# Kernel tuning notes

Measured on AMD Instinct MI355X. Metric: run time of the kernel, lower is better.

The kernel has to match this reference:

```python
import jax, jax.numpy as jnp
import numpy as np

N, S, E = 8, 1024, 768
H = 12
D = E // H  # head_dim = 64
FF = 4 * E
EPS = 1e-5


def setup_inputs() -> dict:
    key = jax.random.key(0)
    ks = jax.random.split(key, 12)
    s = lambda fan_in: 1.0 / np.sqrt(fan_in)
    return {
        "x": jax.random.normal(ks[0], (N, S, E), dtype=jnp.float32),
        "ln1_g": jnp.ones((E,), jnp.float32),
        "ln1_b": jnp.zeros((E,), jnp.float32),
        "ln2_g": jnp.ones((E,), jnp.float32),
        "ln2_b": jnp.zeros((E,), jnp.float32),
        "w_attn": jax.random.normal(ks[1], (E, 3 * E), jnp.float32) * s(E),
        "b_attn": jax.random.normal(ks[2], (3 * E,), jnp.float32) * 0.02,
        "w_proj": jax.random.normal(ks[3], (E, E), jnp.float32) * s(E),
        "b_proj": jax.random.normal(ks[4], (E,), jnp.float32) * 0.02,
        "w_fc": jax.random.normal(ks[5], (E, FF), jnp.float32) * s(E),
        "b_fc": jax.random.normal(ks[6], (FF,), jnp.float32) * 0.02,
        "w_fc2": jax.random.normal(ks[7], (FF, E), jnp.float32) * s(FF),
        "b_fc2": jax.random.normal(ks[8], (E,), jnp.float32) * 0.02,
    }


def _layernorm(x, g, b):
    mu = jnp.mean(x, axis=-1, keepdims=True)
    var = jnp.var(x, axis=-1, keepdims=True)
    return (x - mu) * jax.lax.rsqrt(var + EPS) * g + b


def reference(x, ln1_g, ln1_b, ln2_g, ln2_b, w_attn, b_attn, w_proj, b_proj,
              w_fc, b_fc, w_fc2, b_fc2):
    # --- attention branch (pre-LN) ---
    h = _layernorm(x, ln1_g, ln1_b)
    qkv = h @ w_attn + b_attn                       # [N,S,3E]
    q, k, v = jnp.split(qkv, 3, axis=-1)
    q = q.reshape(N, S, H, D).transpose(0, 2, 1, 3)  # [N,H,S,D]
    k = k.reshape(N, S, H, D).transpose(0, 2, 1, 3)
    v = v.reshape(N, S, H, D).transpose(0, 2, 1, 3)
    attn = jnp.einsum('nhsd,nhtd->nhst', q, k) * (1.0 / np.sqrt(D))
    causal = jnp.tril(jnp.ones((S, S), bool))
    attn = jnp.where(causal, attn, -jnp.inf)
    p = jax.nn.softmax(attn, axis=-1)
    out = jnp.einsum('nhst,nhtd->nhsd', p, v)        # [N,H,S,D]
    out = out.transpose(0, 2, 1, 3).reshape(N, S, E)
    x = x + (out @ w_proj + b_proj)
    # --- MLP branch ---
    h2 = _layernorm(x, ln2_g, ln2_b)
    ff = jax.nn.gelu(h2 @ w_fc + b_fc, approximate=False)  # exact GELU (torch nn.GELU default)
    x = x + (ff @ w_fc2 + b_fc2)
    return x
```

## Files before the change

kernel.cpp:

```cpp
#include <hip/hip_runtime.h>
#include <hip/hip_bf16.h>
#include <stdint.h>

#define S_LEN 1024
#define E_DIM 768
#define H_N   12
#define FF_DIM 3072

typedef __hip_bfloat16 bf16;
using short8  = __attribute__((ext_vector_type(8))) short;
using short4v = __attribute__((ext_vector_type(4))) short;
using f32x4   = __attribute__((ext_vector_type(4))) float;

__device__ __forceinline__ void async_cp16(const void* g, void* l) {
  __builtin_amdgcn_global_load_lds(
      (__attribute__((address_space(1))) void*)(g),
      (__attribute__((address_space(3))) void*)(l), 16, 0, 0);
}

__global__ __launch_bounds__(256) void wcastT_all(
    const float* __restrict__ wa, const float* __restrict__ wp,
    const float* __restrict__ wf, const float* __restrict__ wf2,
    bf16* __restrict__ oa, bf16* __restrict__ op,
    bf16* __restrict__ of, bf16* __restrict__ of2) {
  __shared__ float t[32][33];
  int bid = blockIdx.x;
  const float* w; bf16* wt; int K, N, bx, by;
  if (bid < 1728)      { w = wa;  wt = oa;  K = 768;  N = 2304; int r = bid;        bx = r % 72; by = r / 72; }
  else if (bid < 2304) { w = wp;  wt = op;  K = 768;  N = 768;  int r = bid - 1728; bx = r % 24; by = r / 24; }
  else if (bid < 4608) { w = wf;  wt = of;  K = 768;  N = 3072; int r = bid - 2304; bx = r % 96; by = r / 96; }
  else                 { w = wf2; wt = of2; K = 3072; N = 768;  int r = bid - 4608; bx = r % 24; by = r / 24; }
  int x = threadIdx.x & 31;
  int y = threadIdx.x >> 5;
  for (int i = y; i < 32; i += 8)
    t[i][x] = w[(size_t)(by * 32 + i) * N + bx * 32 + x];
  __syncthreads();
  for (int i = y; i < 32; i += 8)
    wt[(size_t)(bx * 32 + i) * K + by * 32 + x] = __float2bfloat16(t[x][i]);
}

__global__ __launch_bounds__(256) void ln_rows(const float* __restrict__ x,
                                               const float* __restrict__ g,
                                               const float* __restrict__ b,
                                               bf16* __restrict__ out) {
  int row = blockIdx.x;
  int tid = threadIdx.x;
  const float* xr = x + (size_t)row * E_DIM;
  float v0 = xr[tid], v1 = xr[tid + 256], v2 = xr[tid + 512];
  float s = v0 + v1 + v2;
  float ss = v0 * v0 + v1 * v1 + v2 * v2;
  for (int o = 32; o > 0; o >>= 1) {
    s  += __shfl_down(s, o);
    ss += __shfl_down(ss, o);
  }
  __shared__ float ps[4], pq[4];
  int wv = tid >> 6;
  if ((tid & 63) == 0) { ps[wv] = s; pq[wv] = ss; }
  __syncthreads();
  s  = ps[0] + ps[1] + ps[2] + ps[3];
  ss = pq[0] + pq[1] + pq[2] + pq[3];
  float mu  = s * (1.0f / E_DIM);
  float var = ss * (1.0f / E_DIM) - mu * mu;
  float rs  = rsqrtf(var + 1e-5f);
  bf16* orow = out + (size_t)row * E_DIM;
  orow[tid]       = __float2bfloat16((v0 - mu) * rs * g[tid]       + b[tid]);
  orow[tid + 256] = __float2bfloat16((v1 - mu) * rs * g[tid + 256] + b[tid + 256]);
  orow[tid + 512] = __float2bfloat16((v2 - mu) * rs * g[tid + 512] + b[tid + 512]);
}

template <int MODE>
__global__ __launch_bounds__(256) void gemm_bt(
    const bf16* __restrict__ A, const bf16* __restrict__ Bt,
    const float* __restrict__ bias, const float* __restrict__ resid,
    float* __restrict__ outf, bf16* __restrict__ ob0, bf16* __restrict__ ob1,
    bf16* __restrict__ ob2, int M, int N, int K) {
  __shared__ bf16 As[2][128 * 64];
  __shared__ bf16 Bs[2][128 * 64];
  int tid = threadIdx.x;
  int wave = tid >> 6, lane = tid & 63;
  int quad = lane >> 4, l16 = lane & 15;
  int gx = N >> 7;
  int flat = blockIdx.x;
  int y8 = flat & 7;
  int q2 = flat >> 3;
  int bx = q2 % gx;
  int by = (q2 / gx) * 8 + y8;
  int m0 = by * 128, n0 = bx * 128;
  int wm = (wave & 1) * 64, wn = (wave >> 1) * 64;
  f32x4 acc[4][4];
  for (int i = 0; i < 4; i++)
    for (int j = 0; j < 4; j++)
      for (int r = 0; r < 4; r++) acc[i][j][r] = 0.f;

  int xs = l16 & 7;
  int srow = tid >> 3;
  int scg = (((tid & 7) ^ (srow & 7)) << 3);
  const bf16* aptr = A  + (size_t)(m0 + srow) * K + scg;
  const bf16* bptr = Bt + (size_t)(n0 + srow) * K + scg;
  int ldst = tid * 8;

#pragma unroll
  for (int t = 0; t < 4; t++) {
    async_cp16(aptr + (size_t)t * 32 * K, &As[0][ldst + t * 2048]);
    async_cp16(bptr + (size_t)t * 32 * K, &Bs[0][ldst + t * 2048]);
  }
  int nkb = K >> 6;
  for (int ik = 0; ik < nkb; ++ik) {
    int cur = ik & 1;
    if (ik + 1 < nkb) {
      size_t ko = (size_t)(ik + 1) * 64;
#pragma unroll
      for (int t = 0; t < 4; t++) {
        async_cp16(aptr + ko + (size_t)t * 32 * K, &As[cur ^ 1][ldst + t * 2048]);
        async_cp16(bptr + ko + (size_t)t * 32 * K, &Bs[cur ^ 1][ldst + t * 2048]);
      }
      asm volatile("s_waitcnt vmcnt(8)" ::: "memory");
    } else {
      asm volatile("s_waitcnt vmcnt(0)" ::: "memory");
    }
    __builtin_amdgcn_s_barrier();
    asm volatile("" ::: "memory");
#pragma unroll
    for (int ks = 0; ks < 2; ks++) {
      int ko2 = (((ks * 4 + quad) ^ xs) << 3);
      short8 af[4], bfr[4];
      for (int i = 0; i < 4; i++)
        af[i] = *(const short8*)&As[cur][(wm + i * 16 + l16) * 64 + ko2];
      for (int j = 0; j < 4; j++)
        bfr[j] = *(const short8*)&Bs[cur][(wn + j * 16 + l16) * 64 + ko2];
      for (int i = 0; i < 4; i++)
        for (int j = 0; j < 4; j++)
          acc[i][j] = __builtin_amdgcn_mfma_f32_16x16x32_bf16(
              bfr[j], af[i], acc[i][j], 0, 0, 0);
    }
    asm volatile("" ::: "memory");
    __builtin_amdgcn_s_barrier();
  }

  for (int j = 0; j < 4; j++) {
    int colb = n0 + wn + j * 16 + quad * 4;
    f32x4 b4 = *(const f32x4*)&bias[colb];
    for (int i = 0; i < 4; i++) {
      int row = m0 + wm + i * 16 + l16;
      f32x4 v = acc[i][j] + b4;
      if (MODE == 0) {
        int nn = row >> 10, s = row & 1023;
        if (colb < 768) {
          int h = colb >> 6, db = colb & 63;
          short4v pk;
          for (int r = 0; r < 4; r++)
            pk[r] = __builtin_bit_cast(short, __float2bfloat16(v[r] * 0.125f));
          *(short4v*)&ob0[(((size_t)nn * H_N + h) * S_LEN + s) * 64 + db] = pk;
        } else if (colb < 1536) {
          int c = colb - 768;
          size_t nh2 = (size_t)nn * H_N + (c >> 6);
          int d = c & 63;
          short4v pk;
          for (int r = 0; r < 4; r++)
            pk[r] = __builtin_bit_cast(short, __float2bfloat16(v[r]));
          *(short4v*)&ob1[((nh2 * 8 + (d >> 3)) * S_LEN + s) * 8 + (d & 7)] = pk;
        } else {
          int c = colb - 1536;
          size_t nh2 = (size_t)nn * H_N + (c >> 6);
          int d0 = c & 63;
          for (int r = 0; r < 4; r++)
            ob2[((nh2 * 128 + (s >> 3)) * 64 + d0 + r) * 8 + (s & 7)] =
                __float2bfloat16(v[r]);
        }
      } else if (MODE == 2) {
        short4v pk;
        for (int r = 0; r < 4; r++) {
          float x = v[r];
          float t = x * (1.59576912161f + 0.0713548162726f * x * x);
          float g = x * __builtin_amdgcn_rcpf(1.0f + __expf(-t));
          pk[r] = __builtin_bit_cast(short, __float2bfloat16(g));
        }
        *(short4v*)&ob0[(size_t)row * N + colb] = pk;
      }
    }
  }
}

__global__ __launch_bounds__(256) void gemm_bt64(
    const bf16* __restrict__ A, const bf16* __restrict__ Bt,
    const float* __restrict__ bias, const float* __restrict__ resid,
    float* __restrict__ outf, int M, int N, int K) {
  __shared__ bf16 As[2][128 * 64];
  __shared__ bf16 Bs[2][64 * 64];
  int tid = threadIdx.x;
  int wave = tid >> 6, lane = tid & 63;
  int quad = lane >> 4, l16 = lane & 15;
  int gx = N >> 6;
  int flat = blockIdx.x;
  int y8 = flat & 7;
  int q2 = flat >> 3;
  int bx = q2 % gx;
  int by = (q2 / gx) * 8 + y8;
  int m0 = by * 128, n0 = bx * 64;
  int wm = wave * 32;
  f32x4 acc[2][4];
  for (int i = 0; i < 2; i++)
    for (int j = 0; j < 4; j++)
      for (int r = 0; r < 4; r++) acc[i][j][r] = 0.f;

  int xs = l16 & 7;
  int srow = tid >> 3;
  int scg = (((tid & 7) ^ (srow & 7)) << 3);
  const bf16* aptr = A  + (size_t)(m0 + srow) * K + scg;
  const bf16* bptr = Bt + (size_t)(n0 + srow) * K + scg;
  int ldst = tid * 8;

#pragma unroll
  for (int t = 0; t < 4; t++)
    async_cp16(aptr + (size_t)t * 32 * K, &As[0][ldst + t * 2048]);
#pragma unroll
  for (int t = 0; t < 2; t++)
    async_cp16(bptr + (size_t)t * 32 * K, &Bs[0][ldst + t * 2048]);

  int nkb = K >> 6;
  for (int ik = 0; ik < nkb; ++ik) {
    int cur = ik & 1;
    if (ik + 1 < nkb) {
      size_t ko = (size_t)(ik + 1) * 64;
#pragma unroll
      for (int t = 0; t < 4; t++)
        async_cp16(aptr + ko + (size_t)t * 32 * K, &As[cur ^ 1][ldst + t * 2048]);
#pragma unroll
      for (int t = 0; t < 2; t++)
        async_cp16(bptr + ko + (size_t)t * 32 * K, &Bs[cur ^ 1][ldst + t * 2048]);
      asm volatile("s_waitcnt vmcnt(6)" ::: "memory");
    } else {
      asm volatile("s_waitcnt vmcnt(0)" ::: "memory");
    }
    __builtin_amdgcn_s_barrier();
    asm volatile("" ::: "memory");
#pragma unroll
    for (int ks = 0; ks < 2; ks++) {
      int ko2 = (((ks * 4 + quad) ^ xs) << 3);
      short8 af[2], bfr[4];
      for (int i = 0; i < 2; i++)
        af[i] = *(const short8*)&As[cur][(wm + i * 16 + l16) * 64 + ko2];
      for (int j = 0; j < 4; j++)
        bfr[j] = *(const short8*)&Bs[cur][(j * 16 + l16) * 64 + ko2];
      for (int i = 0; i < 2; i++)
        for (int j = 0; j < 4; j++)
          acc[i][j] = __builtin_amdgcn_mfma_f32_16x16x32_bf16(
              bfr[j], af[i], acc[i][j], 0, 0, 0);
    }
    asm volatile("" ::: "memory");
    __builtin_amdgcn_s_barrier();
  }

  for (int j = 0; j < 4; j++) {
    int colb = n0 + j * 16 + quad * 4;
    f32x4 b4 = *(const f32x4*)&bias[colb];
    for (int i = 0; i < 2; i++) {
      int row = m0 + wm + i * 16 + l16;
      size_t idx = (size_t)row * N + colb;
      f32x4 rv = *(const f32x4*)&resid[idx];
      *(f32x4*)&outf[idx] = acc[i][j] + b4 + rv;
    }
  }
}

__global__ __launch_bounds__(256) void attn_fwd(
    const bf16* __restrict__ q, const bf16* __restrict__ kg,
    const bf16* __restrict__ vg, bf16* __restrict__ out) {
  __shared__ bf16 kt2[2][8 * 64 * 8];
  __shared__ bf16 vt2[2][8 * 64 * 8];
  __shared__ bf16 pba[4][16 * 68];
  __shared__ bf16 pbb[4][16 * 68];
  int flat = blockIdx.x;
  int xcd = flat & 7;
  int j = flat >> 3;
  int a = j & 7;
  int g = j >> 3;
  int nh = xcd * 12 + g;
  int b = 15 - a;
  int n = nh / H_N, h = nh % H_N;
  int tid = threadIdx.x, wave = tid >> 6, lane = tid & 63;
  int quad = lane >> 4, l16 = lane & 15;
  const bf16* qp = q  + (size_t)nh * S_LEN * 64;
  const bf16* kp = kg + (size_t)nh * 8 * S_LEN * 8;
  const bf16* vp = vg + (size_t)nh * 128 * 64 * 8;
  int qra = a * 64 + wave * 16;
  int qrb = b * 64 + wave * 16;

  short8 qfa[2], qfb[2];
  qfa[0] = *(const short8*)&qp[(size_t)(qra + l16) * 64 + quad * 8];
  qfa[1] = *(const short8*)&qp[(size_t)(qra + l16) * 64 + 32 + quad * 8];
  qfb[0] = *(const short8*)&qp[(size_t)(qrb + l16) * 64 + quad * 8];
  qfb[1] = *(const short8*)&qp[(size_t)(qrb + l16) * 64 + 32 + quad * 8];

  const bf16* kbase = kp + (((size_t)(tid >> 6) * S_LEN) + (tid & 63)) * 8;
  const bf16* vbase = vp + (((size_t)(tid >> 6) * 64) + (tid & 63)) * 8;

  f32x4 oaa[4], oab[4];
  for (int dt = 0; dt < 4; dt++)
    for (int r = 0; r < 4; r++) { oaa[dt][r] = 0.f; oab[dt][r] = 0.f; }
  float lia = 0.f, lib = 0.f;

  {
    bf16* lk = &kt2[0][0] + tid * 8;
    bf16* lv = &vt2[0][0] + tid * 8;
#pragma unroll
    for (int t = 0; t < 2; ++t) {
      async_cp16(kbase + (size_t)t * 4 * S_LEN * 8, lk + t * 2048);
      async_cp16(vbase + (size_t)t * 2048, lv + t * 2048);
    }
  }

  for (int kb = 0; kb <= b; ++kb) {
    bool act_a = (kb <= a);
    int cur = kb & 1;
    __syncthreads();

    short8 kf[2][4], vf[2][4];
#pragma unroll
    for (int ks = 0; ks < 2; ks++)
      for (int nt = 0; nt < 4; nt++) {
        kf[ks][nt] = *(const short8*)
            &kt2[cur][(size_t)((ks * 4 + quad) * 64 + nt * 16 + l16) * 8];
        vf[ks][nt] = *(const short8*)
            &vt2[cur][(size_t)((ks * 4 + quad) * 64 + nt * 16 + l16) * 8];
      }
    if (kb < b) {
      bf16* lk = &kt2[cur ^ 1][0] + tid * 8;
      bf16* lv = &vt2[cur ^ 1][0] + tid * 8;
      size_t kko = (size_t)(kb + 1) * 512;
      size_t vko = (size_t)(kb + 1) * 4096;
#pragma unroll
      for (int t = 0; t < 2; ++t) {
        async_cp16(kbase + kko + (size_t)t * 4 * S_LEN * 8, lk + t * 2048);
        async_cp16(vbase + vko + (size_t)t * 2048, lv + t * 2048);
      }
    }

    f32x4 sb4[4], sa4[4];
    for (int nt = 0; nt < 4; nt++) {
      for (int r = 0; r < 4; r++) { sb4[nt][r] = -10.f; sa4[nt][r] = -10.f; }
      for (int ks = 0; ks < 2; ks++) {
        sb4[nt] = __builtin_amdgcn_mfma_f32_16x16x32_bf16(kf[ks][nt], qfb[ks],
                                                          sb4[nt], 0, 0, 0);
        if (act_a)
          sa4[nt] = __builtin_amdgcn_mfma_f32_16x16x32_bf16(kf[ks][nt], qfa[ks],
                                                            sa4[nt], 0, 0, 0);
      }
    }
    if (kb == b) {
      int ql = wave * 16 + l16;
      for (int nt = 0; nt < 4; nt++)
        for (int r = 0; r < 4; r++)
          if (nt * 16 + quad * 4 + r > ql) sb4[nt][r] = -INFINITY;
    }
    if (kb == a) {
      int ql = wave * 16 + l16;
      for (int nt = 0; nt < 4; nt++)
        for (int r = 0; r < 4; r++)
          if (nt * 16 + quad * 4 + r > ql) sa4[nt][r] = -INFINITY;
    }

    float rsb = 0.f;
    for (int nt = 0; nt < 4; nt++)
      for (int r = 0; r < 4; r++) {
        float p = __expf(sb4[nt][r]);
        sb4[nt][r] = p;
        rsb += p;
      }
    rsb += __shfl_xor(rsb, 16);
    rsb += __shfl_xor(rsb, 32);
    lib += rsb;
    bf16* pwb = pbb[wave];
    for (int nt = 0; nt < 4; nt++) {
      short4v pk;
      for (int r = 0; r < 4; r++)
        pk[r] = __builtin_bit_cast(short, __float2bfloat16(sb4[nt][r]));
      *(short4v*)&pwb[l16 * 68 + nt * 16 + quad * 4] = pk;
    }
    if (act_a) {
      float rsa = 0.f;
      for (int nt = 0; nt < 4; nt++)
        for (int r = 0; r < 4; r++) {
          float p = __expf(sa4[nt][r]);
          sa4[nt][r] = p;
          rsa += p;
        }
      rsa += __shfl_xor(rsa, 16);
      rsa += __shfl_xor(rsa, 32);
      lia += rsa;
      bf16* pwa = pba[wave];
      for (int nt = 0; nt < 4; nt++) {
        short4v pk;
        for (int r = 0; r < 4; r++)
          pk[r] = __builtin_bit_cast(short, __float2bfloat16(sa4[nt][r]));
        *(short4v*)&pwa[l16 * 68 + nt * 16 + quad * 4] = pk;
      }
    }
    asm volatile("s_waitcnt lgkmcnt(0)" ::: "memory");

    for (int ks = 0; ks < 2; ks++) {
      short8 pfb = *(const short8*)&pbb[wave][l16 * 68 + ks * 32 + quad * 8];
      short8 pfa;
      if (act_a) pfa = *(const short8*)&pba[wave][l16 * 68 + ks * 32 + quad * 8];
      for (int dt = 0; dt < 4; dt++) {
        oab[dt] = __builtin_amdgcn_mfma_f32_16x16x32_bf16(vf[ks][dt], pfb,
                                                          oab[dt], 0, 0, 0);
        if (act_a)
          oaa[dt] = __builtin_amdgcn_mfma_f32_16x16x32_bf16(vf[ks][dt], pfa,
                                                            oaa[dt], 0, 0, 0);
      }
    }
  }

  float inva = 1.0f / lia, invb = 1.0f / lib;
  int ta = n * S_LEN + qra + l16;
  int tb = n * S_LEN + qrb + l16;
  for (int dt = 0; dt < 4; dt++) {
    short4v ova, ovb;
    for (int r = 0; r < 4; r++) {
      ova[r] = __builtin_bit_cast(short, __float2bfloat16(oaa[dt][r] * inva));
      ovb[r] = __builtin_bit_cast(short, __float2bfloat16(oab[dt][r] * invb));
    }
    *(short4v*)&out[(size_t)ta * E_DIM + h * 64 + dt * 16 + quad * 4] = ova;
    *(short4v*)&out[(size_t)tb * E_DIM + h * 64 + dt * 16 + quad * 4] = ovb;
  }
}

extern "C" void kernel_launch(void* const* d_in, const int* in_sizes, int n_in,
                              void* d_out, int out_size, void* d_ws, size_t ws_size,
                              hipStream_t stream) {
  (void)in_sizes; (void)n_in; (void)out_size; (void)ws_size;
  const float* x      = (const float*)d_in[0];
  const float* ln1_g  = (const float*)d_in[1];
  const float* ln1_b  = (const float*)d_in[2];
  const float* ln2_g  = (const float*)d_in[3];
  const float* ln2_b  = (const float*)d_in[4];
  const float* w_attn = (const float*)d_in[5];
  const float* b_attn = (const float*)d_in[6];
  const float* w_proj = (const float*)d_in[7];
  const float* b_proj = (const float*)d_in[8];
  const float* w_fc   = (const float*)d_in[9];
  const float* b_fc   = (const float*)d_in[10];
  const float* w_fc2  = (const float*)d_in[11];
  const float* b_fc2  = (const float*)d_in[12];
  float* out = (float*)d_out;

  char* ws = (char*)d_ws;
  bf16* wt_attn = (bf16*)(ws);
  bf16* wt_proj = (bf16*)(ws + 3538944);
  bf16* wt_fc   = (bf16*)(ws + 4718592);
  bf16* wt_fc2  = (bf16*)(ws + 9437184);
  bf16* hbuf    = (bf16*)(ws + 14155776);
  float* x2     = (float*)(ws + 26738688);
  bf16* qb      = (bf16*)(ws + 51904512);
  bf16* kbuf    = (bf16*)(ws + 64487424);
  bf16* vtb     = (bf16*)(ws + 77070336);
  bf16* ao      = (bf16*)(ws + 89653248);
  bf16* ff      = qb;

  dim3 blk(256);
  wcastT_all<<<dim3(6912), blk, 0, stream>>>(w_attn, w_proj, w_fc, w_fc2,
                                             wt_attn, wt_proj, wt_fc, wt_fc2);

  ln_rows<<<8192, blk, 0, stream>>>(x, ln1_g, ln1_b, hbuf);

  gemm_bt<0><<<dim3(18 * 64), blk, 0, stream>>>(
      hbuf, wt_attn, b_attn, nullptr, nullptr, qb, kbuf, vtb, 8192, 2304, 768);

  attn_fwd<<<dim3(768), blk, 0, stream>>>(qb, kbuf, vtb, ao);

  gemm_bt64<<<dim3(12 * 64), blk, 0, stream>>>(
      ao, wt_proj, b_proj, x, x2, 8192, 768, 768);

  ln_rows<<<8192, blk, 0, stream>>>(x2, ln2_g, ln2_b, hbuf);

  gemm_bt<2><<<dim3(24 * 64), blk, 0, stream>>>(
      hbuf, wt_fc, b_fc, nullptr, nullptr, ff, nullptr, nullptr, 8192, 3072, 768);

  gemm_bt64<<<dim3(12 * 64), blk, 0, stream>>>(
      ff, wt_fc2, b_fc2, x2, out, 8192, 768, 3072);
}
```

Baseline: 349.3 us.

## Replace QKV and FC1 GEMMs with 256x256-tile 8-wave ping-pong pipelined kernel

The 128x128 4-wave GEMM used for the QKV and FC1 projections is replaced by a 256x256-tile kernel with 512 threads. Each wave computes a 128x64 sub-tile. The K loop is split into quarter-tile phases that interleave LDS fragment loads, async global-to-LDS prefetch of the next K slices, and MFMA bursts under raised priority. The larger tile increases data reuse per LDS byte and the schedule is meant to overlap memory with compute. The cost is more barriers, higher register pressure from 128 accumulators per lane, and fewer blocks, 288 and 384, across the CUs.

```diff
diff --git a/kernel.cpp b/kernel.cpp
--- a/kernel.cpp
+++ b/kernel.cpp
@@ -69,80 +69,132 @@
 }
 
 template <int MODE>
-__global__ __launch_bounds__(256) void gemm_bt(
+__global__ __launch_bounds__(512, 2) void gemm8(
     const bf16* __restrict__ A, const bf16* __restrict__ Bt,
-    const float* __restrict__ bias, const float* __restrict__ resid,
-    float* __restrict__ outf, bf16* __restrict__ ob0, bf16* __restrict__ ob1,
-    bf16* __restrict__ ob2, int M, int N, int K) {
-  __shared__ bf16 As[2][128 * 64];
-  __shared__ bf16 Bs[2][128 * 64];
+    const float* __restrict__ bias,
+    bf16* __restrict__ ob0, bf16* __restrict__ ob1, bf16* __restrict__ ob2,
+    int M, int N, int K) {
+  __shared__ bf16 lA[2][16384];
+  __shared__ bf16 lB[2][16384];
   int tid = threadIdx.x;
-  int wave = tid >> 6, lane = tid & 63;
+  int w = tid >> 6, lane = tid & 63;
   int quad = lane >> 4, l16 = lane & 15;
-  int gx = N >> 7;
+  int wr = w >> 2, wc = w & 3;
+  int gx = N >> 8;
   int flat = blockIdx.x;
   int y8 = flat & 7;
   int q2 = flat >> 3;
   int bx = q2 % gx;
   int by = (q2 / gx) * 8 + y8;
-  int m0 = by * 128, n0 = bx * 128;
-  int wm = (wave & 1) * 64, wn = (wave >> 1) * 64;
-  f32x4 acc[4][4];
-  for (int i = 0; i < 4; i++)
+  int m0 = by << 8, n0 = bx << 8;
+
+  f32x4 acc[8][4];
+#pragma unroll
+  for (int i = 0; i < 8; i++)
+#pragma unroll
     for (int j = 0; j < 4; j++)
+#pragma unroll
       for (int r = 0; r < 4; r++) acc[i][j][r] = 0.f;
 
   int xs = l16 & 7;
-  int srow = tid >> 3;
-  int scg = (((tid & 7) ^ (srow & 7)) << 3);
-  const bf16* aptr = A  + (size_t)(m0 + srow) * K + scg;
-  const bf16* bptr = Bt + (size_t)(n0 + srow) * K + scg;
-  int ldst = tid * 8;
-
-#pragma unroll
-  for (int t = 0; t < 4; t++) {
-    async_cp16(aptr + (size_t)t * 32 * K, &As[0][ldst + t * 2048]);
-    async_cp16(bptr + (size_t)t * 32 * K, &Bs[0][ldst + t * 2048]);
-  }
-  int nkb = K >> 6;
-  for (int ik = 0; ik < nkb; ++ik) {
-    int cur = ik & 1;
-    if (ik + 1 < nkb) {
-      size_t ko = (size_t)(ik + 1) * 64;
-#pragma unroll
-      for (int t = 0; t < 4; t++) {
-        async_cp16(aptr + ko + (size_t)t * 32 * K, &As[cur ^ 1][ldst + t * 2048]);
-        async_cp16(bptr + ko + (size_t)t * 32 * K, &Bs[cur ^ 1][ldst + t * 2048]);
-      }
-      asm volatile("s_waitcnt vmcnt(8)" ::: "memory");
-    } else {
-      asm volatile("s_waitcnt vmcnt(0)" ::: "memory");
-    }
-    __builtin_amdgcn_s_barrier();
-    asm volatile("" ::: "memory");
-#pragma unroll
-    for (int ks = 0; ks < 2; ks++) {
-      int ko2 = (((ks * 4 + quad) ^ xs) << 3);
-      short8 af[4], bfr[4];
-      for (int i = 0; i < 4; i++)
-        af[i] = *(const short8*)&As[cur][(wm + i * 16 + l16) * 64 + ko2];
-      for (int j = 0; j < 4; j++)
-        bfr[j] = *(const short8*)&Bs[cur][(wn + j * 16 + l16) * 64 + ko2];
-      for (int i = 0; i < 4; i++)
-        for (int j = 0; j < 4; j++)
-          acc[i][j] = __builtin_amdgcn_mfma_f32_16x16x32_bf16(
-              bfr[j], af[i], acc[i][j], 0, 0, 0);
-    }
-    asm volatile("" ::: "memory");
-    __builtin_amdgcn_s_barrier();
-  }
-
-  for (int j = 0; j < 4; j++) {
-    int colb = n0 + wn + j * 16 + quad * 4;
+  int ko0 = (quad ^ xs) << 3;
+  int ko1 = ((4 + quad) ^ xs) << 3;
+  int sgo = ((tid & 7) ^ ((tid >> 3) & 7)) << 3;
+  size_t aRB = (size_t)(m0 + (tid >> 3)) * K + sgo;
+  size_t bRB = (size_t)(n0 + ((tid >> 8) << 6) + ((tid >> 3) & 31)) * K + sgo;
+  int aD = tid * 8;
+  int bD = ((tid >> 8) << 12) + (tid & 255) * 8;
+
+  auto stA = [&](int buf, int mh, int kt) {
+#pragma unroll
+    for (int p = 0; p < 2; ++p)
+      async_cp16(A + aRB + (size_t)(mh * 64 + p * 128) * K + (size_t)kt * 64,
+                 &lA[buf][aD + mh * 4096 + p * 8192]);
+  };
+  auto stB = [&](int buf, int nh, int kt) {
+#pragma unroll
+    for (int p = 0; p < 2; ++p)
+      async_cp16(Bt + bRB + (size_t)(nh * 32 + p * 128) * K + (size_t)kt * 64,
+                 &lB[buf][bD + nh * 2048 + p * 8192]);
+  };
+
+  short8 af[4][2], b0f[2][2], b1f[2][2];
+
+#define LD_A(BUF, MH)                                                      \
+  {                                                                        \
+    _Pragma("unroll") for (int i = 0; i < 4; ++i) {                        \
+      const bf16* bp = &lA[BUF][(wr * 128 + (MH)*64 + i * 16 + l16) * 64]; \
+      af[i][0] = *(const short8*)&bp[ko0];                                 \
+      af[i][1] = *(const short8*)&bp[ko1];                                 \
+    }                                                                      \
+  }
+#define LD_B(BUF, NH, DST)                                                 \
+  {                                                                        \
+    _Pragma("unroll") for (int j = 0; j < 2; ++j) {                        \
+      const bf16* bp = &lB[BUF][(wc * 64 + (NH)*32 + j * 16 + l16) * 64];  \
+      DST[j][0] = *(const short8*)&bp[ko0];                                \
+      DST[j][1] = *(const short8*)&bp[ko1];                                \
+    }                                                                      \
+  }
+#define DO_MFMA(MH, NH, BSRC)                                              \
+  {                                                                        \
+    __builtin_amdgcn_s_setprio(1);                                         \
+    _Pragma("unroll") for (int ks = 0; ks < 2; ++ks)                       \
+        _Pragma("unroll") for (int i = 0; i < 4; ++i)                      \
+            _Pragma("unroll") for (int j = 0; j < 2; ++j)                  \
+                acc[(MH)*4 + i][(NH)*2 + j] =                              \
+        __builtin_amdgcn_mfma_f32_16x16x32_bf16(                           \
+            BSRC[j][ks], af[i][ks], acc[(MH)*4 + i][(NH)*2 + j], 0, 0, 0); \
+    __builtin_amdgcn_s_setprio(0);                                         \
+  }
+#define BAR() __builtin_amdgcn_s_barrier()
+#define LGKM0() asm volatile("s_waitcnt lgkmcnt(0)" ::: "memory")
+#define VM6() asm volatile("s_waitcnt vmcnt(6)" ::: "memory")
+#define VM0() asm volatile("s_waitcnt vmcnt(0)" ::: "memory")
+
+  stA(0, 0, 0); stA(0, 1, 0); stB(0, 0, 0); stB(0, 1, 0);
+  stA(1, 0, 1); stB(1, 1, 1); stA(1, 1, 1);
+  VM6();
+  BAR();
+
+  int nit = K >> 7;
+  for (int it = 0; it < nit; ++it) {
+    int kt1 = 2 * it + 1, ktA = 2 * it + 2, ktB = 2 * it + 3;
+    bool more = (it + 1 < nit);
+    LD_A(0, 0); LD_B(0, 0, b0f);
+    stB(1, 0, kt1);
+    BAR(); LGKM0(); DO_MFMA(0, 0, b0f); BAR();
+    LD_B(0, 1, b1f);
+    if (more) stA(0, 0, ktA);
+    BAR(); LGKM0(); DO_MFMA(0, 1, b1f); BAR();
+    LD_A(0, 1);
+    if (more) stB(0, 1, ktA);
+    BAR(); LGKM0(); DO_MFMA(1, 1, b1f); BAR();
+    LD_B(0, 0, b0f);
+    if (more) { stA(0, 1, ktA); VM6(); } else { VM0(); }
+    BAR(); LGKM0(); DO_MFMA(1, 0, b0f); BAR();
+    LD_A(1, 0); LD_B(1, 0, b0f);
+    if (more) stB(0, 0, ktA);
+    BAR(); LGKM0(); DO_MFMA(0, 0, b0f); BAR();
+    LD_B(1, 1, b1f);
+    if (more) stA(1, 0, ktB);
+    BAR(); LGKM0(); DO_MFMA(0, 1, b1f); BAR();
+    LD_A(1, 1);
+    if (more) stB(1, 1, ktB);
+    BAR(); LGKM0(); DO_MFMA(1, 1, b1f); BAR();
+    LD_B(1, 0, b0f);
+    if (more) { stA(1, 1, ktB); VM6(); }
+    BAR(); LGKM0(); DO_MFMA(1, 0, b0f); BAR();
+  }
+
+#pragma unroll
+  for (int nj = 0; nj < 4; ++nj) {
+    int colb = n0 + wc * 64 + nj * 16 + quad * 4;
     f32x4 b4 = *(const f32x4*)&bias[colb];
-    for (int i = 0; i < 4; i++) {
-      int row = m0 + wm + i * 16 + l16;
-      f32x4 v = acc[i][j] + b4;
+#pragma unroll
+    for (int mi = 0; mi < 8; ++mi) {
+      int row = m0 + wr * 128 + mi * 16 + l16;
+      f32x4 v = acc[mi][nj] + b4;
       if (MODE == 0) {
         int nn = row >> 10, s = row & 1023;
         if (colb < 768) {
@@ -179,6 +231,13 @@
       }
     }
   }
+#undef LD_A
+#undef LD_B
+#undef DO_MFMA
+#undef BAR
+#undef LGKM0
+#undef VM6
+#undef VM0
 }
 
 __global__ __launch_bounds__(256) void gemm_bt64(
@@ -464,8 +523,8 @@
 
   ln_rows<<<8192, blk, 0, stream>>>(x, ln1_g, ln1_b, hbuf);
 
-  gemm_bt<0><<<dim3(18 * 64), blk, 0, stream>>>(
-      hbuf, wt_attn, b_attn, nullptr, nullptr, qb, kbuf, vtb, 8192, 2304, 768);
+  gemm8<0><<<dim3(288), dim3(512), 0, stream>>>(
+      hbuf, wt_attn, b_attn, qb, kbuf, vtb, 8192, 2304, 768);
 
   attn_fwd<<<dim3(768), blk, 0, stream>>>(qb, kbuf, vtb, ao);
 
@@ -474,8 +533,8 @@
 
   ln_rows<<<8192, blk, 0, stream>>>(x2, ln2_g, ln2_b, hbuf);
 
-  gemm_bt<2><<<dim3(24 * 64), blk, 0, stream>>>(
-      hbuf, wt_fc, b_fc, nullptr, nullptr, ff, nullptr, nullptr, 8192, 3072, 768);
+  gemm8<2><<<dim3(384), dim3(512), 0, stream>>>(
+      hbuf, wt_fc, b_fc, ff, nullptr, nullptr, 8192, 3072, 768);
 
   gemm_bt64<<<dim3(12 * 64), blk, 0, stream>>>(
       ff, wt_fc2, b_fc2, x2, out, 8192, 768, 3072);
```

Measured after the change: 367.5 us. 1.05x slower.
